# Performance work log

Measured on AMD Instinct MI355X. Metric: run time of the kernel, lower is better.

## Reference

```python
import jax, jax.numpy as jnp
import numpy as np

N = 100000      # nodes
E = 1600000     # edges
D_IN = 128      # input_dim
H = 256         # hidden_dim
L = 3           # num_layers
B = 64          # graphs per batch
BN_EPS = 1e-5


def setup_inputs() -> dict:
    key = jax.random.key(0)
    ks = jax.random.split(key, 8)
    x = jax.random.normal(ks[0], (N, D_IN), dtype=jnp.float32)
    edge_index = jax.random.randint(ks[1], (2, E), 0, N, dtype=jnp.int32)
    batch = jnp.sort(jax.random.randint(ks[2], (N,), 0, B, dtype=jnp.int32))
    W0 = jax.random.normal(ks[3], (D_IN, H), dtype=jnp.float32) / np.sqrt(D_IN)
    W_rest = jax.random.normal(ks[4], (L - 1, H, H), dtype=jnp.float32) / np.sqrt(H)
    b = jax.random.normal(ks[5], (L, H), dtype=jnp.float32) * 0.01
    gamma = 1.0 + jax.random.normal(ks[6], (L, H), dtype=jnp.float32) * 0.01
    beta = jax.random.normal(ks[7], (L, H), dtype=jnp.float32) * 0.01
    return {"x": x, "W0": W0, "W_rest": W_rest, "b": b, "gamma": gamma,
            "beta": beta, "edge_index": edge_index, "batch": batch}


def reference(x, W0, W_rest, b, gamma, beta, edge_index, batch):
    src, dst = edge_index[0], edge_index[1]
    # GCN symmetric normalization with self-loops: deg = in-degree + 1
    deg = jax.ops.segment_sum(jnp.ones((E,), x.dtype), dst, num_segments=N) + 1.0
    dis = jax.lax.rsqrt(deg)                   # deg^{-1/2}, [N]
    enorm = dis[src] * dis[dst]                # per-edge norm, [E]
    self_norm = (dis * dis)[:, None]           # self-loop norm = 1/deg, [N,1]

    def gcn_bn_relu(h, W, bb, g, be):
        h = h @ W                                                  # [N,H]
        agg = jax.ops.segment_sum(h[src] * enorm[:, None], dst, num_segments=N)
        h = agg + h * self_norm + bb                               # self-loop + bias
        # BatchNorm1d (training mode: batch stats, biased variance)
        m = h.mean(axis=0)
        v = h.var(axis=0)
        h = (h - m) * jax.lax.rsqrt(v + BN_EPS) * g + be
        return jax.nn.relu(h)                                      # dropout = identity (eval)

    h = gcn_bn_relu(x, W0, b[0], gamma[0], beta[0])
    for i in range(L - 1):
        h = gcn_bn_relu(h, W_rest[i], b[i + 1], gamma[i + 1], beta[i + 1])

    # segment pooling per graph (att_pool in the original is dead code: not returned)
    counts = jax.ops.segment_sum(jnp.ones((N,), h.dtype), batch, num_segments=B)
    mean_pool = jax.ops.segment_sum(h, batch, num_segments=B) / counts[:, None]
    max_pool = jax.ops.segment_max(h, batch, num_segments=B)
    return jnp.concatenate([mean_pool, max_pool], axis=1)          # [B, 2H]
```

## Files before the change

kernel.cpp:

```cpp
#include <hip/hip_runtime.h>
#include <hip/hip_bf16.h>
#include <stdint.h>


#define NN 100000
#define EE 1600000
#define BB 64
#define MPAD 100096
#define NBM (MPAD / 256)

typedef __attribute__((ext_vector_type(8))) short short8;
typedef __attribute__((ext_vector_type(4))) float f32x4;

__device__ __forceinline__ float bflo(uint32_t v){ return __uint_as_float(v << 16); }
__device__ __forceinline__ float bfhi(uint32_t v){ return __uint_as_float(v & 0xffff0000u); }
__device__ __forceinline__ uint32_t bfrne(float x){
  uint32_t u = __float_as_uint(x);
  return (u + 0x7fffu + ((u >> 16) & 1u)) >> 16;
}
__device__ __forceinline__ uint32_t bfpack(float a, float b){ return bfrne(a) | (bfrne(b) << 16); }
__device__ __forceinline__ float phi(long long p){
  return __uint_as_float((uint32_t)((unsigned long long)p >> 32));
}

__device__ __forceinline__ void gload_lds16(const void* g, void* l){
  __builtin_amdgcn_global_load_lds(
      (const __attribute__((address_space(1))) uint32_t*)g,
      (__attribute__((address_space(3))) uint32_t*)l, 16, 0, 0);
}

__global__ void k_deg(const int* __restrict__ dst, int* __restrict__ degi){
  for (int e = blockIdx.x * blockDim.x + threadIdx.x; e < EE; e += gridDim.x * blockDim.x)
    atomicAdd(&degi[dst[e]], 1);
}

__global__ void k_scan1(const int* __restrict__ degi, int* __restrict__ rp, int* __restrict__ bsum,
                        float* __restrict__ dis){
  __shared__ int lds[256];
  int b = blockIdx.x, t = threadIdx.x;
  int base = b * 1024 + t * 4;
  int v0 = (base + 0 < NN) ? degi[base + 0] : 0;
  int v1 = (base + 1 < NN) ? degi[base + 1] : 0;
  int v2 = (base + 2 < NN) ? degi[base + 2] : 0;
  int v3 = (base + 3 < NN) ? degi[base + 3] : 0;
  if (base + 0 < NN) dis[base + 0] = rsqrtf((float)v0 + 1.0f);
  if (base + 1 < NN) dis[base + 1] = rsqrtf((float)v1 + 1.0f);
  if (base + 2 < NN) dis[base + 2] = rsqrtf((float)v2 + 1.0f);
  if (base + 3 < NN) dis[base + 3] = rsqrtf((float)v3 + 1.0f);
  int s = v0 + v1 + v2 + v3;
  lds[t] = s; __syncthreads();
  for (int off = 1; off < 256; off <<= 1){
    int x = (t >= off) ? lds[t - off] : 0; __syncthreads();
    lds[t] += x; __syncthreads();
  }
  int excl = lds[t] - s;
  if (t == 255) bsum[b] = lds[255];
  if (base + 0 < NN) rp[base + 0] = excl;
  if (base + 1 < NN) rp[base + 1] = excl + v0;
  if (base + 2 < NN) rp[base + 2] = excl + v0 + v1;
  if (base + 3 < NN) rp[base + 3] = excl + v0 + v1 + v2;
}

__global__ void k_scan2(int* __restrict__ bsum, int nb){
  if (blockIdx.x == 0 && threadIdx.x == 0){
    int run = 0;
    for (int i = 0; i < nb; ++i){ int t = bsum[i]; bsum[i] = run; run += t; }
  }
}

__global__ void k_scan3(int* __restrict__ rp, int* __restrict__ cursor, const int* __restrict__ bsum){
  int b = blockIdx.x, t = threadIdx.x;
  int add = bsum[b];
  int base = b * 1024 + t * 4;
  #pragma unroll
  for (int j = 0; j < 4; ++j){
    int i = base + j;
    if (i < NN){ int v = rp[i] + add; rp[i] = v; cursor[i] = v; }
  }
  if (b == 0 && t == 0) rp[NN] = EE;
}

__global__ void k_fill(const int* __restrict__ src, const int* __restrict__ dst,
                       const float* __restrict__ dis, int* __restrict__ cursor,
                       long long* __restrict__ cp){
  for (int e = blockIdx.x * blockDim.x + threadIdx.x; e < EE; e += gridDim.x * blockDim.x){
    int s = src[e], d = dst[e];
    int pos = atomicAdd(&cursor[d], 1);
    float nrm = dis[s] * dis[d];
    long long v = (long long)(unsigned int)s | ((long long)(unsigned int)__float_as_uint(nrm) << 32);
    cp[pos] = v;
  }
}

__global__ void k_sort(const int* __restrict__ rp, long long* __restrict__ cp){
  int row = blockIdx.x * 256 + threadIdx.x;
  if (row >= NN) return;
  int beg = rp[row], end = rp[row + 1];
  for (int i = beg + 1; i < end; ++i){
    long long key = cp[i];
    int j = i - 1;
    while (j >= beg && cp[j] > key){ cp[j + 1] = cp[j]; --j; }
    cp[j + 1] = key;
  }
}

__global__ void k_wtall(const float* __restrict__ W0, const float* __restrict__ Wr,
                        uint16_t* __restrict__ Wt0, uint16_t* __restrict__ Wt1,
                        uint16_t* __restrict__ Wt2){
  int i = blockIdx.x * 256 + threadIdx.x;
  if (i < 32768){
    int c = i >> 7, k = i & 127;
    Wt0[i] = (uint16_t)bfrne(W0[k * 256 + c]);
  } else if (i < 32768 + 131072){
    int j = i - 32768;
    int m = j >> 16, jj = j & 65535;
    int c = jj >> 8, k = jj & 255;
    uint16_t v = (uint16_t)bfrne(Wr[m * 65536 + k * 256 + c]);
    if (m == 0) Wt1[jj] = v; else Wt2[jj] = v;
  }
}

__global__ void k_cvtx(const float* __restrict__ x, uint32_t* __restrict__ Xb){
  int i = blockIdx.x * 256 + threadIdx.x;
  if (i >= MPAD * 64) return;
  int row = i >> 6;
  uint32_t r = 0u;
  if (row < NN){
    int col = (i & 63) * 2;
    r = bfpack(x[row * 128 + col], x[row * 128 + col + 1]);
  }
  Xb[i] = r;
}

__global__ void k_agg256(const uint2* __restrict__ Xin, const int* __restrict__ rp,
                         const long long* __restrict__ cp, const float* __restrict__ dis,
                         uint2* __restrict__ Xout){
  int lane = threadIdx.x & 63;
  int slot = threadIdx.x >> 6;
  int row0 = blockIdx.x * 16 + slot;
  for (int rr = 0; rr < 4; ++rr){
    int row = row0 + rr * 4;
    if (row >= NN){
      if (row < MPAD){ uint2 z = {0u, 0u}; Xout[(size_t)row * 64 + lane] = z; }
      continue;
    }
    int beg = rp[row], end = rp[row + 1];
    float a0 = 0.f, a1 = 0.f, a2 = 0.f, a3 = 0.f;
    int e = beg;
    for (; e + 8 <= end; e += 8){
      long long p[8]; uint2 v[8];
      #pragma unroll
      for (int u = 0; u < 8; ++u) p[u] = cp[e + u];
      #pragma unroll
      for (int u = 0; u < 8; ++u) v[u] = Xin[(size_t)(int)p[u] * 64 + lane];
      #pragma unroll
      for (int u = 0; u < 8; ++u){
        float w = phi(p[u]);
        a0 += w * bflo(v[u].x); a1 += w * bfhi(v[u].x);
        a2 += w * bflo(v[u].y); a3 += w * bfhi(v[u].y);
      }
    }
    for (; e < end; ++e){
      long long p0 = cp[e];
      float w = phi(p0);
      uint2 v = Xin[(size_t)(int)p0 * 64 + lane];
      a0 += w * bflo(v.x); a1 += w * bfhi(v.x);
      a2 += w * bflo(v.y); a3 += w * bfhi(v.y);
    }
    float dv = dis[row]; float sn = dv * dv;
    uint2 vs = Xin[(size_t)row * 64 + lane];
    a0 += sn * bflo(vs.x); a1 += sn * bfhi(vs.x);
    a2 += sn * bflo(vs.y); a3 += sn * bfhi(vs.y);
    uint2 o; o.x = bfpack(a0, a1); o.y = bfpack(a2, a3);
    Xout[(size_t)row * 64 + lane] = o;
  }
}

__global__ void k_agg128(const uint2* __restrict__ Xin, const int* __restrict__ rp,
                         const long long* __restrict__ cp, const float* __restrict__ dis,
                         uint2* __restrict__ Xout){
  int lane = threadIdx.x & 63;
  int half = lane >> 5, j = lane & 31;
  int slot = threadIdx.x >> 6;
  int row0 = blockIdx.x * 16 + slot;
  for (int rr = 0; rr < 4; ++rr){
    int row = row0 + rr * 4;
    if (row >= NN){
      if (row < MPAD && half == 0){ uint2 z = {0u, 0u}; Xout[(size_t)row * 32 + j] = z; }
      continue;
    }
    int beg = rp[row], end = rp[row + 1];
    float a0 = 0.f, a1 = 0.f, a2 = 0.f, a3 = 0.f;
    int e = beg;
    for (; e + 8 <= end; e += 8){
      long long p[4]; uint2 v[4];
      #pragma unroll
      for (int u = 0; u < 4; ++u) p[u] = cp[e + u * 2 + half];
      #pragma unroll
      for (int u = 0; u < 4; ++u) v[u] = Xin[(size_t)(int)p[u] * 32 + j];
      #pragma unroll
      for (int u = 0; u < 4; ++u){
        float w = phi(p[u]);
        a0 += w * bflo(v[u].x); a1 += w * bfhi(v[u].x);
        a2 += w * bflo(v[u].y); a3 += w * bfhi(v[u].y);
      }
    }
    for (; e < end; e += 2){
      int idx = e + half;
      bool ok = idx < end;
      long long p0 = cp[ok ? idx : end - 1];
      float w = ok ? phi(p0) : 0.f;
      uint2 v = Xin[(size_t)(int)p0 * 32 + j];
      a0 += w * bflo(v.x); a1 += w * bfhi(v.x);
      a2 += w * bflo(v.y); a3 += w * bfhi(v.y);
    }
    a0 += __shfl_xor(a0, 32); a1 += __shfl_xor(a1, 32);
    a2 += __shfl_xor(a2, 32); a3 += __shfl_xor(a3, 32);
    if (half == 0){
      float dv = dis[row]; float sn = dv * dv;
      uint2 vs = Xin[(size_t)row * 32 + j];
      a0 += sn * bflo(vs.x); a1 += sn * bfhi(vs.x);
      a2 += sn * bflo(vs.y); a3 += sn * bfhi(vs.y);
      uint2 o; o.x = bfpack(a0, a1); o.y = bfpack(a2, a3);
      Xout[(size_t)row * 32 + j] = o;
    }
  }
}

template<int K>
__global__ __launch_bounds__(512) void k_gemm(const uint16_t* __restrict__ A,
                                              const uint16_t* __restrict__ Bt,
                                              uint32_t* __restrict__ Cb,
                                              float* __restrict__ pstat){
  __shared__ __align__(16) uint16_t lA[2][8192];
  __shared__ __align__(16) uint16_t lB[2][4096];
  __shared__ float lp[8][128];
  int tid = threadIdx.x;
  int l = tid & 63;
  int bm = blockIdx.x, bn = blockIdx.y;

  f32x4 acc[4][4];
  #pragma unroll
  for (int m = 0; m < 4; ++m)
    #pragma unroll
    for (int n = 0; n < 4; ++n){ f32x4 z = {0.f,0.f,0.f,0.f}; acc[m][n] = z; }

  int w = tid >> 6, wr = w >> 1, wc = w & 1;
  int rbase = wr * 64, cbase = wc * 64;
  int lrow = l & 15, lk8 = l >> 4;

  auto stage = [&](int kt, int buf){
    #pragma unroll
    for (int i = 0; i < 2; ++i){
      int c = i * 512 + tid;
      int k8 = c >> 8, r = c & 255;
      size_t ga = (size_t)(bm * 256 + r) * K + kt * 32 + k8 * 8;
      gload_lds16((const char*)(A + ga), (char*)&lA[buf][c * 8]);
    }
    int k8b = tid >> 7, rb = tid & 127;
    size_t gb = (size_t)(bn * 128 + rb) * K + kt * 32 + k8b * 8;
    gload_lds16((const char*)(Bt + gb), (char*)&lB[buf][tid * 8]);
  };

  stage(0, 0);
  __syncthreads();
  constexpr int NT = K / 32;
  for (int kt = 0; kt < NT; ++kt){
    int cur = kt & 1;
    if (kt + 1 < NT) stage(kt + 1, cur ^ 1);
    short8 afr[4], bfr[4];
    #pragma unroll
    for (int m = 0; m < 4; ++m)
      afr[m] = *(const short8*)&lA[cur][(lk8 * 256 + rbase + m * 16 + lrow) * 8];
    #pragma unroll
    for (int n = 0; n < 4; ++n)
      bfr[n] = *(const short8*)&lB[cur][(lk8 * 128 + cbase + n * 16 + lrow) * 8];
    #pragma unroll
    for (int m = 0; m < 4; ++m)
      #pragma unroll
      for (int n = 0; n < 4; ++n)
        acc[m][n] = __builtin_amdgcn_mfma_f32_16x16x32_bf16(afr[m], bfr[n], acc[m][n], 0, 0, 0);
    __syncthreads();
  }

  int grow0 = bm * 256 + rbase + (l >> 4) * 4;
  int gcol0 = bn * 128 + cbase + (l & 15);
  uint16_t* C16 = (uint16_t*)Cb;
  float sa[4] = {0.f,0.f,0.f,0.f}, sb[4] = {0.f,0.f,0.f,0.f};
  #pragma unroll
  for (int m = 0; m < 4; ++m){
    #pragma unroll
    for (int n = 0; n < 4; ++n){
      int col = gcol0 + n * 16;
      int r0 = grow0 + m * 16;
      f32x4 v = acc[m][n];
      #pragma unroll
      for (int q = 0; q < 4; ++q){
        C16[(size_t)(r0 + q) * 256 + col] = (uint16_t)bfrne(v[q]);
        sa[n] += v[q]; sb[n] += v[q] * v[q];
      }
    }
  }
  #pragma unroll
  for (int n = 0; n < 4; ++n){
    sa[n] += __shfl_xor(sa[n], 16); sa[n] += __shfl_xor(sa[n], 32);
    sb[n] += __shfl_xor(sb[n], 16); sb[n] += __shfl_xor(sb[n], 32);
  }
  if (l < 16){
    #pragma unroll
    for (int n = 0; n < 4; ++n){
      lp[w][n * 16 + l] = sa[n];
      lp[w][64 + n * 16 + l] = sb[n];
    }
  }
  __syncthreads();
  if (tid < 256){
    int kind = tid >> 7, c = tid & 127;
    int wc2 = c >> 6, cc = c & 63;
    float v = lp[wc2][kind * 64 + cc] + lp[2 + wc2][kind * 64 + cc]
            + lp[4 + wc2][kind * 64 + cc] + lp[6 + wc2][kind * 64 + cc];
    pstat[(size_t)(bm * 2 + bn) * 256 + kind * 128 + c] = v;
  }
}

__global__ void k_finalize(const float* __restrict__ pstat, const float* __restrict__ gamma,
                           const float* __restrict__ beta, float* __restrict__ ss){
  int c = threadIdx.x;
  int bn = c >> 7, lc = c & 127;
  double s = 0., s2 = 0.;
  for (int bm = 0; bm < NBM; ++bm){
    const float* p = pstat + (size_t)(bm * 2 + bn) * 256;
    s  += (double)p[lc];
    s2 += (double)p[128 + lc];
  }
  double mean = s / (double)NN;
  double var  = s2 / (double)NN - mean * mean;
  float rstd = rsqrtf((float)var + 1e-5f);
  float sc = gamma[c] * rstd;
  ss[c] = sc;
  ss[256 + c] = beta[c] - (float)mean * sc;
}

__global__ void k_bnapply(const uint4* __restrict__ Y, const float* __restrict__ ss,
                          uint4* __restrict__ X){
  int i = blockIdx.x * 256 + threadIdx.x;
  if (i >= MPAD * 32) return;
  uint4 v = Y[i];
  int c0 = (i & 31) * 8;
  float r0 = fmaxf(bflo(v.x) * ss[c0 + 0] + ss[256 + c0 + 0], 0.f);
  float r1 = fmaxf(bfhi(v.x) * ss[c0 + 1] + ss[256 + c0 + 1], 0.f);
  float r2 = fmaxf(bflo(v.y) * ss[c0 + 2] + ss[256 + c0 + 2], 0.f);
  float r3 = fmaxf(bfhi(v.y) * ss[c0 + 3] + ss[256 + c0 + 3], 0.f);
  float r4 = fmaxf(bflo(v.z) * ss[c0 + 4] + ss[256 + c0 + 4], 0.f);
  float r5 = fmaxf(bfhi(v.z) * ss[c0 + 5] + ss[256 + c0 + 5], 0.f);
  float r6 = fmaxf(bflo(v.w) * ss[c0 + 6] + ss[256 + c0 + 6], 0.f);
  float r7 = fmaxf(bfhi(v.w) * ss[c0 + 7] + ss[256 + c0 + 7], 0.f);
  uint4 o;
  o.x = bfpack(r0, r1); o.y = bfpack(r2, r3);
  o.z = bfpack(r4, r5); o.w = bfpack(r6, r7);
  X[i] = o;
}

__global__ void k_segstart(const int* __restrict__ batch, int* __restrict__ seg){
  int g = threadIdx.x;
  if (g > BB) return;
  if (g == BB){ seg[BB] = NN; return; }
  int lo = 0, hi = NN;
  while (lo < hi){ int mid = (lo + hi) >> 1; if (batch[mid] < g) lo = mid + 1; else hi = mid; }
  seg[g] = lo;
}

__global__ void k_poolpart(const uint32_t* __restrict__ X, const int* __restrict__ seg,
                           float* __restrict__ pb){
  int g = blockIdx.x, c = blockIdx.y, t = threadIdx.x;
  int s = seg[g], e = seg[g + 1];
  int len = e - s;
  int c0 = s + (int)(((long long)len * c) >> 3);
  int c1 = s + (int)(((long long)len * (c + 1)) >> 3);
  float sm0 = 0.f, sm1 = 0.f, mx0 = -1e30f, mx1 = -1e30f;
  #pragma unroll 4
  for (int r = c0; r < c1; ++r){
    uint32_t v = X[(size_t)r * 128 + t];
    float a = bflo(v), b2 = bfhi(v);
    sm0 += a; sm1 += b2;
    mx0 = fmaxf(mx0, a); mx1 = fmaxf(mx1, b2);
  }
  float* p = pb + (size_t)(g * 8 + c) * 512;
  p[2 * t] = sm0; p[2 * t + 1] = sm1;
  p[256 + 2 * t] = mx0; p[256 + 2 * t + 1] = mx1;
}

__global__ void k_poolred(const float* __restrict__ pb, const int* __restrict__ seg,
                          float* __restrict__ out){
  int g = blockIdx.x, cc = threadIdx.x;
  float s = 0.f, m = -1e30f;
  #pragma unroll
  for (int c = 0; c < 8; ++c){
    const float* p = pb + (size_t)(g * 8 + c) * 512;
    s += p[cc];
    m = fmaxf(m, p[256 + cc]);
  }
  float inv = 1.0f / (float)(seg[g + 1] - seg[g]);
  out[g * 512 + cc] = s * inv;
  out[g * 512 + 256 + cc] = m;
}

extern "C" void kernel_launch(void* const* d_in, const int* in_sizes, int n_in,
                              void* d_out, int out_size, void* d_ws, size_t ws_size,
                              hipStream_t stream){
  const float* x     = (const float*)d_in[0];
  const float* W0    = (const float*)d_in[1];
  const float* Wr    = (const float*)d_in[2];
  const float* gamma = (const float*)d_in[4];
  const float* beta  = (const float*)d_in[5];
  const int*   ei    = (const int*)d_in[6];
  const int*   batch = (const int*)d_in[7];
  const int* esrc = ei;
  const int* edst = ei + EE;
  float* out = (float*)d_out;

  char* base = (char*)d_ws;
  size_t off = 0;
  auto alloc = [&](size_t b)->char*{
    char* p = base + off; off = (off + b + 255) & ~(size_t)255; return p;
  };
  uint32_t* Xbuf = (uint32_t*)alloc((size_t)MPAD * 256 * 2);
  uint32_t* Xagg = (uint32_t*)alloc((size_t)MPAD * 256 * 2);
  uint32_t* Y    = (uint32_t*)alloc((size_t)MPAD * 256 * 2);
  uint16_t* Wt0  = (uint16_t*)alloc(256 * 128 * 2);
  uint16_t* Wt1  = (uint16_t*)alloc(256 * 256 * 2);
  uint16_t* Wt2  = (uint16_t*)alloc(256 * 256 * 2);
  int*   degi   = (int*)  alloc((size_t)NN * 4);
  float* dis    = (float*)alloc((size_t)NN * 4);
  int*   rp     = (int*)  alloc((size_t)(NN + 1) * 4);
  int*   cursor = (int*)  alloc((size_t)NN * 4);
  int*   bsum   = (int*)  alloc(128 * 4);
  long long* cp = (long long*)alloc((size_t)EE * 8);
  float* pstat  = (float*)alloc((size_t)NBM * 2 * 256 * 4);
  float* ss     = (float*)alloc(512 * 4);
  int*   seg    = (int*)  alloc((BB + 1) * 4);
  float* pb     = (float*)alloc((size_t)BB * 8 * 512 * 4);

  hipMemsetAsync(degi, 0, (size_t)NN * 4, stream);
  k_deg<<<2048, 256, 0, stream>>>(edst, degi);
  k_scan1<<<98, 256, 0, stream>>>(degi, rp, bsum, dis);
  k_scan2<<<1, 1, 0, stream>>>(bsum, 98);
  k_scan3<<<98, 256, 0, stream>>>(rp, cursor, bsum);
  k_fill<<<2048, 256, 0, stream>>>(esrc, edst, dis, cursor, cp);
  k_sort<<<(NN + 255) / 256, 256, 0, stream>>>(rp, cp);
  k_wtall<<<640, 256, 0, stream>>>(W0, Wr, Wt0, Wt1, Wt2);
  k_cvtx<<<MPAD * 64 / 256, 256, 0, stream>>>(x, Xbuf);

  k_agg128<<<MPAD / 16, 256, 0, stream>>>((const uint2*)Xbuf, rp, cp, dis, (uint2*)Xagg);
  k_gemm<128><<<dim3(NBM, 2), 512, 0, stream>>>((const uint16_t*)Xagg, Wt0, Y, pstat);
  k_finalize<<<1, 256, 0, stream>>>(pstat, gamma + 0, beta + 0, ss);
  k_bnapply<<<MPAD * 32 / 256, 256, 0, stream>>>((const uint4*)Y, ss, (uint4*)Xbuf);

  k_agg256<<<MPAD / 16, 256, 0, stream>>>((const uint2*)Xbuf, rp, cp, dis, (uint2*)Xagg);
  k_gemm<256><<<dim3(NBM, 2), 512, 0, stream>>>((const uint16_t*)Xagg, Wt1, Y, pstat);
  k_finalize<<<1, 256, 0, stream>>>(pstat, gamma + 256, beta + 256, ss);
  k_bnapply<<<MPAD * 32 / 256, 256, 0, stream>>>((const uint4*)Y, ss, (uint4*)Xbuf);

  k_agg256<<<MPAD / 16, 256, 0, stream>>>((const uint2*)Xbuf, rp, cp, dis, (uint2*)Xagg);
  k_gemm<256><<<dim3(NBM, 2), 512, 0, stream>>>((const uint16_t*)Xagg, Wt2, Y, pstat);
  k_finalize<<<1, 256, 0, stream>>>(pstat, gamma + 512, beta + 512, ss);
  k_bnapply<<<MPAD * 32 / 256, 256, 0, stream>>>((const uint4*)Y, ss, (uint4*)Xbuf);

  k_segstart<<<1, 128, 0, stream>>>(batch, seg);
  k_poolpart<<<dim3(BB, 8), 128, 0, stream>>>(Xbuf, seg, pb);
  k_poolred<<<BB, 256, 0, stream>>>(pb, seg, out);
}
```

Before: 922.0 us.

## Wave-parallel bitonic CSR sort, pipelined gather in agg256, fused segment search

The per-row CSR sort moves from one thread doing insertion sort to one wavefront doing a register bitonic sort via shuffles, keeping a serial fallback for rows with more than 64 edges. The 256-wide aggregation now loads edge records cooperatively and broadcasts them with shuffles, double-buffering two groups of eight neighbour gathers to keep more loads in flight. BN finalize splits its serial double accumulation into eight independent chains, and the segment-start kernel is removed by computing a binary search inside the pooling kernels. Costs are higher register use in the aggregation and repeated binary searches per pooling block.

```diff
diff --git a/kernel.cpp b/kernel.cpp
--- a/kernel.cpp
+++ b/kernel.cpp
@@ -93,14 +93,33 @@
 }
 
 __global__ void k_sort(const int* __restrict__ rp, long long* __restrict__ cp){
-  int row = blockIdx.x * 256 + threadIdx.x;
-  if (row >= NN) return;
-  int beg = rp[row], end = rp[row + 1];
-  for (int i = beg + 1; i < end; ++i){
-    long long key = cp[i];
-    int j = i - 1;
-    while (j >= beg && cp[j] > key){ cp[j + 1] = cp[j]; --j; }
-    cp[j + 1] = key;
+  int wid = (blockIdx.x * blockDim.x + threadIdx.x) >> 6;
+  int lane = threadIdx.x & 63;
+  if (wid >= NN) return;
+  int beg = rp[wid], end = rp[wid + 1];
+  int d = end - beg;
+  if (d <= 1) return;
+  if (d <= 64){
+    long long key = (lane < d) ? cp[beg + lane] : 0x7fffffffffffffffLL;
+    #pragma unroll
+    for (int k = 2; k <= 64; k <<= 1){
+      #pragma unroll
+      for (int j = k >> 1; j > 0; j >>= 1){
+        long long other = __shfl_xor(key, j);
+        bool up = ((lane & k) == 0);
+        bool keepMin = (((lane & j) == 0) == up);
+        bool take = keepMin ? (other < key) : (other > key);
+        if (take) key = other;
+      }
+    }
+    if (lane < d) cp[beg + lane] = key;
+  } else if (lane == 0){
+    for (int i = beg + 1; i < end; ++i){
+      long long k2 = cp[i];
+      int j = i - 1;
+      while (j >= beg && cp[j] > k2){ cp[j + 1] = cp[j]; --j; }
+      cp[j + 1] = k2;
+    }
   }
 }
 
@@ -135,8 +154,10 @@
 __global__ void k_agg256(const uint2* __restrict__ Xin, const int* __restrict__ rp,
                          const long long* __restrict__ cp, const float* __restrict__ dis,
                          uint2* __restrict__ Xout){
+  const uint2* C2 = (const uint2*)cp;
   int lane = threadIdx.x & 63;
   int slot = threadIdx.x >> 6;
+  int g8 = lane & 56;
   int row0 = blockIdx.x * 16 + slot;
   for (int rr = 0; rr < 4; ++rr){
     int row = row0 + rr * 4;
@@ -145,22 +166,54 @@
       continue;
     }
     int beg = rp[row], end = rp[row + 1];
+    int nf = (end - beg) >> 3;
     float a0 = 0.f, a1 = 0.f, a2 = 0.f, a3 = 0.f;
-    int e = beg;
-    for (; e + 8 <= end; e += 8){
-      long long p[8]; uint2 v[8];
-      #pragma unroll
-      for (int u = 0; u < 8; ++u) p[u] = cp[e + u];
-      #pragma unroll
-      for (int u = 0; u < 8; ++u) v[u] = Xin[(size_t)(int)p[u] * 64 + lane];
+    uint2 cA = {0u,0u}, cB = {0u,0u};
+    uint2 vA[8], vB[8];
+
+    if (nf > 0){
+      cA = C2[beg + (lane & 7)];
       #pragma unroll
       for (int u = 0; u < 8; ++u){
-        float w = phi(p[u]);
-        a0 += w * bflo(v[u].x); a1 += w * bfhi(v[u].x);
-        a2 += w * bflo(v[u].y); a3 += w * bfhi(v[u].y);
+        int su = __shfl((int)cA.x, g8 | u);
+        vA[u] = Xin[(size_t)su * 64 + lane];
       }
     }
-    for (; e < end; ++e){
+    if (nf > 1){
+      cB = C2[beg + 8 + (lane & 7)];
+      #pragma unroll
+      for (int u = 0; u < 8; ++u){
+        int su = __shfl((int)cB.x, g8 | u);
+        vB[u] = Xin[(size_t)su * 64 + lane];
+      }
+    }
+
+#define CONSUME(c, v) { \
+    _Pragma("unroll") \
+    for (int u = 0; u < 8; ++u){ \
+      float w = __uint_as_float((uint32_t)__shfl((int)c.y, g8 | u)); \
+      a0 += w * bflo(v[u].x); a1 += w * bfhi(v[u].x); \
+      a2 += w * bflo(v[u].y); a3 += w * bfhi(v[u].y); \
+    } }
+#define REFILL(c, v, pk) if ((pk) < nf){ \
+    c = C2[beg + (pk) * 8 + (lane & 7)]; \
+    _Pragma("unroll") \
+    for (int u = 0; u < 8; ++u){ \
+      int su = __shfl((int)c.x, g8 | u); \
+      v[u] = Xin[(size_t)su * 64 + lane]; \
+    } }
+
+    int it = 0;
+    while (it + 1 < nf){
+      CONSUME(cA, vA); REFILL(cA, vA, it + 2);
+      CONSUME(cB, vB); REFILL(cB, vB, it + 3);
+      it += 2;
+    }
+    if (it < nf){ CONSUME(cA, vA); ++it; }
+#undef CONSUME
+#undef REFILL
+
+    for (int e = beg + nf * 8; e < end; ++e){
       long long p0 = cp[e];
       float w = phi(p0);
       uint2 v = Xin[(size_t)(int)p0 * 64 + lane];
@@ -327,14 +380,27 @@
                            const float* __restrict__ beta, float* __restrict__ ss){
   int c = threadIdx.x;
   int bn = c >> 7, lc = c & 127;
-  double s = 0., s2 = 0.;
-  for (int bm = 0; bm < NBM; ++bm){
+  double s[8], s2[8];
+  #pragma unroll
+  for (int j = 0; j < 8; ++j){ s[j] = 0.; s2[j] = 0.; }
+  int bm = 0;
+  for (; bm + 8 <= NBM; bm += 8){
+    #pragma unroll
+    for (int j = 0; j < 8; ++j){
+      const float* p = pstat + (size_t)((bm + j) * 2 + bn) * 256;
+      s[j]  += (double)p[lc];
+      s2[j] += (double)p[128 + lc];
+    }
+  }
+  for (; bm < NBM; ++bm){
     const float* p = pstat + (size_t)(bm * 2 + bn) * 256;
-    s  += (double)p[lc];
-    s2 += (double)p[128 + lc];
-  }
-  double mean = s / (double)NN;
-  double var  = s2 / (double)NN - mean * mean;
+    s[0]  += (double)p[lc];
+    s2[0] += (double)p[128 + lc];
+  }
+  double S  = ((s[0]+s[1])+(s[2]+s[3]))  + ((s[4]+s[5])+(s[6]+s[7]));
+  double S2 = ((s2[0]+s2[1])+(s2[2]+s2[3])) + ((s2[4]+s2[5])+(s2[6]+s2[7]));
+  double mean = S / (double)NN;
+  double var  = S2 / (double)NN - mean * mean;
   float rstd = rsqrtf((float)var + 1e-5f);
   float sc = gamma[c] * rstd;
   ss[c] = sc;
@@ -361,19 +427,18 @@
   X[i] = o;
 }
 
-__global__ void k_segstart(const int* __restrict__ batch, int* __restrict__ seg){
-  int g = threadIdx.x;
-  if (g > BB) return;
-  if (g == BB){ seg[BB] = NN; return; }
+__device__ __forceinline__ int segfind(const int* __restrict__ batch, int g){
+  if (g <= 0) return 0;
+  if (g >= BB) return NN;
   int lo = 0, hi = NN;
   while (lo < hi){ int mid = (lo + hi) >> 1; if (batch[mid] < g) lo = mid + 1; else hi = mid; }
-  seg[g] = lo;
-}
-
-__global__ void k_poolpart(const uint32_t* __restrict__ X, const int* __restrict__ seg,
+  return lo;
+}
+
+__global__ void k_poolpart(const uint32_t* __restrict__ X, const int* __restrict__ batch,
                            float* __restrict__ pb){
   int g = blockIdx.x, c = blockIdx.y, t = threadIdx.x;
-  int s = seg[g], e = seg[g + 1];
+  int s = segfind(batch, g), e = segfind(batch, g + 1);
   int len = e - s;
   int c0 = s + (int)(((long long)len * c) >> 3);
   int c1 = s + (int)(((long long)len * (c + 1)) >> 3);
@@ -390,7 +455,7 @@
   p[256 + 2 * t] = mx0; p[256 + 2 * t + 1] = mx1;
 }
 
-__global__ void k_poolred(const float* __restrict__ pb, const int* __restrict__ seg,
+__global__ void k_poolred(const float* __restrict__ pb, const int* __restrict__ batch,
                           float* __restrict__ out){
   int g = blockIdx.x, cc = threadIdx.x;
   float s = 0.f, m = -1e30f;
@@ -400,7 +465,7 @@
     s += p[cc];
     m = fmaxf(m, p[256 + cc]);
   }
-  float inv = 1.0f / (float)(seg[g + 1] - seg[g]);
+  float inv = 1.0f / (float)(segfind(batch, g + 1) - segfind(batch, g));
   out[g * 512 + cc] = s * inv;
   out[g * 512 + 256 + cc] = m;
 }
@@ -438,7 +503,6 @@
   long long* cp = (long long*)alloc((size_t)EE * 8);
   float* pstat  = (float*)alloc((size_t)NBM * 2 * 256 * 4);
   float* ss     = (float*)alloc(512 * 4);
-  int*   seg    = (int*)  alloc((BB + 1) * 4);
   float* pb     = (float*)alloc((size_t)BB * 8 * 512 * 4);
 
   hipMemsetAsync(degi, 0, (size_t)NN * 4, stream);
@@ -447,7 +511,7 @@
   k_scan2<<<1, 1, 0, stream>>>(bsum, 98);
   k_scan3<<<98, 256, 0, stream>>>(rp, cursor, bsum);
   k_fill<<<2048, 256, 0, stream>>>(esrc, edst, dis, cursor, cp);
-  k_sort<<<(NN + 255) / 256, 256, 0, stream>>>(rp, cp);
+  k_sort<<<NN / 4, 256, 0, stream>>>(rp, cp);
   k_wtall<<<640, 256, 0, stream>>>(W0, Wr, Wt0, Wt1, Wt2);
   k_cvtx<<<MPAD * 64 / 256, 256, 0, stream>>>(x, Xbuf);
 
@@ -466,7 +530,6 @@
   k_finalize<<<1, 256, 0, stream>>>(pstat, gamma + 512, beta + 512, ss);
   k_bnapply<<<MPAD * 32 / 256, 256, 0, stream>>>((const uint4*)Y, ss, (uint4*)Xbuf);
 
-  k_segstart<<<1, 128, 0, stream>>>(batch, seg);
-  k_poolpart<<<dim3(BB, 8), 128, 0, stream>>>(Xbuf, seg, pb);
-  k_poolred<<<BB, 256, 0, stream>>>(pb, seg, out);
-}
+  k_poolpart<<<dim3(BB, 8), 128, 0, stream>>>(Xbuf, batch, pb);
+  k_poolred<<<BB, 256, 0, stream>>>(pb, batch, out);
+}
```

Result: faster. 868.8 us (-5.8%).
